# Kernel tuning notes

Measured on AMD Instinct MI355X. Metric: run time of the kernel, lower is better.

## Reference

```python
import jax, jax.numpy as jnp
import numpy as np

N_HEADS = 8
TOPK = 64
LN_EPS = 1e-5


def layernorm(x, g, b):
    mu = jnp.mean(x, axis=-1, keepdims=True)
    var = jnp.mean((x - mu) ** 2, axis=-1, keepdims=True)
    return (x - mu) * jax.lax.rsqrt(var + LN_EPS) * g + b


def mha(x, wq, wk, wv, wo, causal):
    # x: [B, S, H]; weights are torch nn.Linear style [out, in]
    B, S, H = x.shape
    hd = H // N_HEADS
    scale = 1.0 / np.sqrt(hd)

    def proj(w):
        return (x @ w.T).reshape(B, S, N_HEADS, hd).transpose(0, 2, 1, 3)  # [B, n, S, hd]

    q, k, v = proj(wq), proj(wk), proj(wv)
    s = jnp.einsum('bnqd,bnkd->bnqk', q, k) * scale
    if causal:
        m = jnp.tril(jnp.ones((S, S), bool))
        s = jnp.where(m, s, jnp.finfo(s.dtype).min)
    a = jax.nn.softmax(s, axis=-1)
    o = jnp.einsum('bnqk,bnkd->bnqd', a, v).transpose(0, 2, 1, 3).reshape(B, S, H)
    return o @ wo.T


def topk_activation(x, k):
    # x: [N, F]; keep top-k per row, zero elsewhere (matches topk + scatter_)
    vals, idx = jax.lax.top_k(x, k)
    rows = jnp.arange(x.shape[0])[:, None]
    return jnp.zeros_like(x).at[rows, idx].set(vals)


def setup_inputs() -> dict:
    key = jax.random.key(0)
    B, D, L, H, F = 8, 16, 128, 512, 4096
    ks = jax.random.split(key, 12)
    s = 1.0 / np.sqrt(H)
    w = lambda k, shp, sc: jax.random.normal(k, shp, jnp.float32) * sc
    return {
        'zL': w(ks[0], (B, D, L, H), 1.0),
        'wq_l': w(ks[1], (H, H), s), 'wk_l': w(ks[2], (H, H), s),
        'wv_l': w(ks[3], (H, H), s), 'wo_l': w(ks[4], (H, H), s),
        'gamma_l': jnp.ones(H, jnp.float32), 'beta_l': jnp.zeros(H, jnp.float32),
        'wq_d': w(ks[5], (H, H), s), 'wk_d': w(ks[6], (H, H), s),
        'wv_d': w(ks[7], (H, H), s), 'wo_d': w(ks[8], (H, H), s),
        'gamma_d': jnp.ones(H, jnp.float32), 'beta_d': jnp.zeros(H, jnp.float32),
        'dict_enc': w(ks[9], (F, H), np.sqrt(2.0 / (H + F))),
        'bias_pre': jnp.zeros(H, jnp.float32),
        'bias_enc': jnp.zeros(F, jnp.float32),
        'query_token': jnp.zeros(H, jnp.float32),
    }


def reference(zL, wq_l, wk_l, wv_l, wo_l, gamma_l, beta_l,
              wq_d, wk_d, wv_d, wo_d, gamma_d, beta_d,
              dict_enc, bias_pre, bias_enc, query_token):
    B, D, L, H = zL.shape
    F = dict_enc.shape[0]
    # prepend learned query token along depth, drop last layer
    qt = jnp.broadcast_to(query_token[None, None, None, :], (B, 1, L, H))
    x = jnp.concatenate([qt, zL[:, :-1, :, :]], axis=1)  # [B, D, L, H]
    # non-causal attention over L within each (b, d)
    x = x.reshape(B * D, L, H)
    x = x + mha(layernorm(x, gamma_l, beta_l), wq_l, wk_l, wv_l, wo_l, causal=False)
    # causal attention over D within each (b, l)
    x = x.reshape(B, D, L, H).transpose(0, 2, 1, 3).reshape(B * L, D, H)
    x = x + mha(layernorm(x, gamma_d, beta_d), wq_d, wk_d, wv_d, wo_d, causal=True)
    x_prior = x.reshape(B, L, D, H).transpose(0, 2, 1, 3)  # [B, D, L, H]
    # dictionary encode on residual (detached in original)
    N = B * D * L
    x_src = jax.lax.stop_gradient(zL - x_prior).reshape(N, H)
    logits = (x_src - bias_pre[None, :]) @ dict_enc.T + bias_enc
    z_dense = jax.nn.relu(logits)
    z_flat = topk_activation(z_dense, TOPK)
    z_n = z_flat.reshape(B, D, L, F)
    return z_n, x_prior
```

## Files before the change

### kernel.cpp

```cpp
#include <hip/hip_runtime.h>
#include <stdint.h>

#define NTOK 16384
#define HDIM 512
#define FDIM 4096
#define NHEAD 8
#define QKVD 1536
#define L2E 1.44269504f

typedef __attribute__((ext_vector_type(8))) _Float16 f16x8;
typedef __attribute__((ext_vector_type(16))) float f32x16;
#define LOSCALE 4096.0f
#define LOINV   (1.0f / 4096.0f)

static __device__ __forceinline__ void ld8f(const float* p, float* v) {
    *(float4*)&v[0] = *(const float4*)p;
    *(float4*)&v[4] = *(const float4*)(p + 4);
}
static __device__ __forceinline__ void st8f(float* p, const float* v) {
    *(float4*)p       = *(const float4*)&v[0];
    *(float4*)(p + 4) = *(const float4*)&v[4];
}

__global__ __launch_bounds__(256) void build_x_k(const float* __restrict__ zL,
                                                 const float* __restrict__ qt,
                                                 float* __restrict__ X) {
    int idx = blockIdx.x * 256 + threadIdx.x;
    int n = idx >> 6;
    int h = (idx & 63) << 3;
    int d = (n >> 7) & 15;
    const float* src = d ? (zL + (((size_t)(n - 128)) << 9) + h) : (qt + h);
    float v[8];
    ld8f(src, v);
    st8f(X + (((size_t)n) << 9) + h, v);
}

__global__ __launch_bounds__(256) void ln_split_k(const float* __restrict__ X,
                                                  const float* __restrict__ gamma,
                                                  const float* __restrict__ beta,
                                                  _Float16* __restrict__ ph,
                                                  _Float16* __restrict__ pl) {
    int row = blockIdx.x * 4 + (threadIdx.x >> 6);
    int lane = threadIdx.x & 63;
    int h = lane << 3;
    const float* xr = X + (((size_t)row) << 9) + h;
    float v[8];
    ld8f(xr, v);
    float s = 0.f;
#pragma unroll
    for (int i = 0; i < 8; ++i) s += v[i];
#pragma unroll
    for (int off = 32; off; off >>= 1) s += __shfl_xor(s, off);
    float m = s * (1.0f / 512.0f);
    float q = 0.f;
#pragma unroll
    for (int i = 0; i < 8; ++i) { float d = v[i] - m; q += d * d; }
#pragma unroll
    for (int off = 32; off; off >>= 1) q += __shfl_xor(q, off);
    float rs = 1.0f / sqrtf(q * (1.0f / 512.0f) + 1e-5f);
    float gv[8], be[8];
    ld8f(gamma + h, gv);
    ld8f(beta + h, be);
    _Float16 h8[8], l8[8];
#pragma unroll
    for (int i = 0; i < 8; ++i) {
        float y = (v[i] - m) * rs * gv[i] + be[i];
        _Float16 hh = (_Float16)y;
        h8[i] = hh;
        l8[i] = (_Float16)((y - (float)hh) * LOSCALE);
    }
    size_t off = (((size_t)row) << 9) + h;
    *(int4*)(ph + off) = *(int4*)h8;
    *(int4*)(pl + off) = *(int4*)l8;
}

__global__ __launch_bounds__(512) void attn_l_k(const float* __restrict__ QKV,
                                                _Float16* __restrict__ xh,
                                                _Float16* __restrict__ xl) {
    __shared__ float ks[64][64];
    __shared__ float vs[64][64];
    const int seq = blockIdx.x, head = blockIdx.y;
    const int t = threadIdx.x;
    const size_t tok0 = (size_t)seq << 7;
    const int ho = head << 6;
    const int r = t >> 2;
    const int q = t & 3;
    const float* qp = QKV + (tok0 + r) * QKVD + ho;
    float qr[16];
#pragma unroll
    for (int i = 0; i < 16; ++i) qr[i] = qp[(i << 2) + q];
    float o[16];
#pragma unroll
    for (int d = 0; d < 16; ++d) o[d] = 0.f;
    float m = -1e30f, l = 0.f;
    for (int half = 0; half < 2; ++half) {
        const int j0 = half << 6;
        __syncthreads();
#pragma unroll
        for (int i = 0; i < 2; ++i) {
            int slot = t + (i << 9);
            int row = slot >> 4;
            int c4 = (slot & 15) << 2;
            size_t g = (tok0 + j0 + row) * QKVD + ho + c4;
            *(float4*)&ks[row][c4] = *(const float4*)(QKV + g + 512);
            *(float4*)&vs[row][c4] = *(const float4*)(QKV + g + 1024);
        }
        __syncthreads();
        for (int j = 0; j < 64; ++j) {
            const float* kp = &ks[j][q];
            float s0 = 0.f, s1 = 0.f, s2 = 0.f, s3 = 0.f;
#pragma unroll
            for (int i = 0; i < 16; i += 4) {
                s0 = fmaf(qr[i + 0], kp[(i + 0) << 2], s0);
                s1 = fmaf(qr[i + 1], kp[(i + 1) << 2], s1);
                s2 = fmaf(qr[i + 2], kp[(i + 2) << 2], s2);
                s3 = fmaf(qr[i + 3], kp[(i + 3) << 2], s3);
            }
            float sp = (s0 + s1) + (s2 + s3);
            sp += __shfl_xor(sp, 1);
            sp += __shfl_xor(sp, 2);
            float s = sp * 0.125f;
            if (s > m) {
                float c = exp2f((m - s) * L2E);
#pragma unroll
                for (int d = 0; d < 16; ++d) o[d] *= c;
                l *= c;
                m = s;
            }
            float w = exp2f((s - m) * L2E);
            l += w;
            const float* vp = &vs[j][q];
#pragma unroll
            for (int i = 0; i < 16; ++i) o[i] = fmaf(w, vp[i << 2], o[i]);
        }
    }
    float inv = 1.0f / l;
    size_t eo = ((tok0 + r) << 9) + ho + q;
#pragma unroll
    for (int i = 0; i < 16; ++i) {
        float y = o[i] * inv;
        _Float16 hh = (_Float16)y;
        xh[eo + (i << 2)] = hh;
        xl[eo + (i << 2)] = (_Float16)((y - (float)hh) * LOSCALE);
    }
}

__global__ __launch_bounds__(128) void attn_d_k(const float* __restrict__ QKV,
                                                _Float16* __restrict__ xh,
                                                _Float16* __restrict__ xl) {
    __shared__ float ks[16][512];
    __shared__ float vs[16][512];
    const int bl = blockIdx.x;
    const int b = bl >> 7, l = bl & 127;
    const int t = threadIdx.x;
    const size_t tok0 = (size_t)b * 2048 + l;
#pragma unroll
    for (int i = 0; i < 16; ++i) {
        int c4 = t << 2;
        int hc = c4 >> 6;
        int p  = (c4 & ~63) | ((c4 + (hc << 2)) & 63);
        size_t g = (tok0 + (size_t)i * 128) * QKVD + c4;
        *(float4*)&ks[i][p] = *(const float4*)(QKV + g + 512);
        *(float4*)&vs[i][p] = *(const float4*)(QKV + g + 1024);
    }
    __syncthreads();
    const int head = t >> 4, dr = t & 15;
    const int ho = head << 6;
    const int rot = head << 2;
    float qr[64];
    const float* qp = QKV + (tok0 + (size_t)dr * 128) * QKVD + ho;
#pragma unroll
    for (int i = 0; i < 16; ++i) *(float4*)&qr[i << 2] = *(const float4*)(qp + (i << 2));
    float s[16];
    float m = -1e30f;
#pragma unroll
    for (int j = 0; j < 16; ++j) {
        float s0 = 0.f, s1 = 0.f, s2 = 0.f, s3 = 0.f;
#pragma unroll
        for (int d = 0; d < 64; d += 4) {
            s0 = fmaf(qr[d + 0], ks[j][ho + ((d + 0 + rot) & 63)], s0);
            s1 = fmaf(qr[d + 1], ks[j][ho + ((d + 1 + rot) & 63)], s1);
            s2 = fmaf(qr[d + 2], ks[j][ho + ((d + 2 + rot) & 63)], s2);
            s3 = fmaf(qr[d + 3], ks[j][ho + ((d + 3 + rot) & 63)], s3);
        }
        float sv = ((s0 + s1) + (s2 + s3)) * 0.125f;
        s[j] = (j <= dr) ? sv : -1e30f;
        m = fmaxf(m, s[j]);
    }
    float lsum = 0.f;
#pragma unroll
    for (int j = 0; j < 16; ++j) {
        float w = (j <= dr) ? exp2f((s[j] - m) * L2E) : 0.f;
        s[j] = w;
        lsum += w;
    }
    float inv = 1.0f / lsum;
    float o[64];
#pragma unroll
    for (int d = 0; d < 64; ++d) o[d] = 0.f;
#pragma unroll
    for (int j = 0; j < 16; ++j) {
        float w = s[j];
#pragma unroll
        for (int d = 0; d < 64; ++d) o[d] = fmaf(w, vs[j][ho + ((d + rot) & 63)], o[d]);
    }
    size_t eo = ((tok0 + (size_t)dr * 128) << 9) + ho;
#pragma unroll
    for (int i = 0; i < 8; ++i) {
        _Float16 h8[8], l8[8];
#pragma unroll
        for (int j = 0; j < 8; ++j) {
            float y = o[i * 8 + j] * inv;
            _Float16 hh = (_Float16)y;
            h8[j] = hh;
            l8[j] = (_Float16)((y - (float)hh) * LOSCALE);
        }
        *(int4*)(xh + eo + (i << 3)) = *(int4*)h8;
        *(int4*)(xl + eo + (i << 3)) = *(int4*)l8;
    }
}

__global__ __launch_bounds__(256) void xprior_xsrc_k(const float* __restrict__ zL,
                                                     const float* __restrict__ bias_pre,
                                                     const float* __restrict__ X,
                                                     float* __restrict__ out_xp,
                                                     _Float16* __restrict__ xh,
                                                     _Float16* __restrict__ xl) {
    int idx = blockIdx.x * 256 + threadIdx.x;
    int h = (idx & 63) << 3;
    size_t off = ((size_t)idx) << 3;
    float z[8], p[8], x[8];
    ld8f(zL + off, z);
    ld8f(bias_pre + h, p);
    ld8f(X + off, x);
    st8f(out_xp + off, x);
    _Float16 h8[8], l8[8];
#pragma unroll
    for (int i = 0; i < 8; ++i) {
        float y = z[i] - x[i] - p[i];
        _Float16 hh = (_Float16)y;
        h8[i] = hh;
        l8[i] = (_Float16)((y - (float)hh) * LOSCALE);
    }
    *(int4*)(xh + off) = *(int4*)h8;
    *(int4*)(xl + off) = *(int4*)l8;
}

__global__ __launch_bounds__(256) void split2_k(const float* __restrict__ in,
                                                _Float16* __restrict__ ph,
                                                _Float16* __restrict__ pl) {
    int idx = blockIdx.x * 256 + threadIdx.x;
    float v[8];
    ld8f(in + (((size_t)idx) << 3), v);
    _Float16 h8[8], l8[8];
#pragma unroll
    for (int i = 0; i < 8; ++i) {
        _Float16 h = (_Float16)v[i];
        float r = v[i] - (float)h;
        h8[i] = h;
        l8[i] = (_Float16)(r * LOSCALE);
    }
    *(int4*)(ph + (((size_t)idx) << 3)) = *(int4*)h8;
    *(int4*)(pl + (((size_t)idx) << 3)) = *(int4*)l8;
}

#define LDT 34
template<int SWZ, bool ADD_C, bool BIAS>
__global__ __launch_bounds__(256) void gemm_f16_k(
        const _Float16* __restrict__ Xh, const _Float16* __restrict__ Xl,
        const _Float16* __restrict__ Wh, const _Float16* __restrict__ Wl,
        const float* __restrict__ bias, float* __restrict__ Cout, int ldc) {
    __shared__ _Float16 Ah[2][128][LDT], Al[2][128][LDT];
    __shared__ _Float16 Bh[2][64][LDT],  Bl[2][64][LDT];
    const int tid = threadIdx.x;
    int bm, bn;
    if (SWZ) {
        int id = blockIdx.x;
        int xcd = id & 7, ww = id >> 3;
        bn = ((xcd << 3) | (ww & 7)) << 6;
        bm = (ww >> 3) << 7;
    } else {
        bm = blockIdx.y << 7;
        bn = blockIdx.x << 6;
    }
    const int w = tid >> 6, lane = tid & 63;
    const int wr = w >> 1, wc = w & 1;
    const int l31 = lane & 31, hh = lane >> 5;
    const int ar0 = tid >> 2, akg = (tid & 3) << 3;
    const int ar1 = ar0 + 64;
    const _Float16* pXh0 = Xh + (size_t)(bm + ar0) * HDIM + akg;
    const _Float16* pXl0 = Xl + (size_t)(bm + ar0) * HDIM + akg;
    const _Float16* pXh1 = Xh + (size_t)(bm + ar1) * HDIM + akg;
    const _Float16* pXl1 = Xl + (size_t)(bm + ar1) * HDIM + akg;
    const _Float16* pWh  = Wh + (size_t)(bn + ar0) * HDIM + akg;
    const _Float16* pWl  = Wl + (size_t)(bn + ar0) * HDIM + akg;

    f32x16 acc1[2], acc2[2];
#pragma unroll
    for (int i = 0; i < 2; ++i)
#pragma unroll
        for (int r = 0; r < 16; ++r) { acc1[i][r] = 0.f; acc2[i][r] = 0.f; }

    int4 ra0h, ra0l, ra1h, ra1l, rbh, rbl;
    auto LOADR = [&](int k0) {
        ra0h = *(const int4*)(pXh0 + k0);
        ra0l = *(const int4*)(pXl0 + k0);
        ra1h = *(const int4*)(pXh1 + k0);
        ra1l = *(const int4*)(pXl1 + k0);
        rbh  = *(const int4*)(pWh + k0);
        rbl  = *(const int4*)(pWl + k0);
    };
    auto STORE = [&](int buf) {
        *(int4*)&Ah[buf][ar0][akg] = ra0h;
        *(int4*)&Al[buf][ar0][akg] = ra0l;
        *(int4*)&Ah[buf][ar1][akg] = ra1h;
        *(int4*)&Al[buf][ar1][akg] = ra1l;
        *(int4*)&Bh[buf][ar0][akg] = rbh;
        *(int4*)&Bl[buf][ar0][akg] = rbl;
    };

    LOADR(0);
    STORE(0);
    int cur = 0;
    for (int it = 0; it < 16; ++it) {
        if (it < 15) LOADR((it + 1) << 5);
        __syncthreads();
#pragma unroll
        for (int kh = 0; kh < 2; ++kh) {
            const int ko = (kh << 4) + (hh << 3);
            f16x8 fah[2], fal[2];
#pragma unroll
            for (int mf = 0; mf < 2; ++mf) {
                int ar = (wr << 6) + (mf << 5) + l31;
                fah[mf] = *(const f16x8*)&Ah[cur][ar][ko];
                fal[mf] = *(const f16x8*)&Al[cur][ar][ko];
            }
            int bc_ = (wc << 5) + l31;
            f16x8 bh = *(const f16x8*)&Bh[cur][bc_][ko];
            f16x8 bl = *(const f16x8*)&Bl[cur][bc_][ko];
#pragma unroll
            for (int mf = 0; mf < 2; ++mf) {
                acc1[mf] = __builtin_amdgcn_mfma_f32_32x32x16_f16(fah[mf], bh, acc1[mf], 0, 0, 0);
                acc2[mf] = __builtin_amdgcn_mfma_f32_32x32x16_f16(fah[mf], bl, acc2[mf], 0, 0, 0);
                acc2[mf] = __builtin_amdgcn_mfma_f32_32x32x16_f16(fal[mf], bh, acc2[mf], 0, 0, 0);
            }
        }
        if (it < 15) { STORE(cur ^ 1); cur ^= 1; }
    }
    const int col = bn + (wc << 5) + l31;
    const float badd = BIAS ? bias[col] : 0.f;
#pragma unroll
    for (int mf = 0; mf < 2; ++mf) {
#pragma unroll
        for (int r = 0; r < 16; ++r) {
            int row = bm + (wr << 6) + (mf << 5) + (r & 3) + ((r >> 2) << 3) + (hh << 2);
            float* cp = Cout + (size_t)row * ldc + col;
            float val = acc1[mf][r] + acc2[mf][r] * LOINV + badd;
            if (ADD_C) val += *cp;
            *cp = val;
        }
    }
}

__global__ __launch_bounds__(256) void topk_k(const float* __restrict__ logits,
                                              float* __restrict__ out) {
    const int row = blockIdx.x;
    const float* lr = logits + (((size_t)row) << 12);
    const int t = threadIdx.x;
    float v[16]; uint32_t u[16];
#pragma unroll
    for (int i = 0; i < 16; ++i) {
        float x = fmaxf(lr[t + (i << 8)], 0.f);
        v[i] = x;
        u[i] = __float_as_uint(x);
    }
    __shared__ int red[4];
    __shared__ unsigned long long bits[64];
    __shared__ int s_cut;
    uint32_t prefix = 0;
    bool exact = false;
    for (int bit = 30; bit >= 0; --bit) {
        uint32_t c = prefix | (1u << bit);
        int cnt = 0;
#pragma unroll
        for (int i = 0; i < 16; ++i) cnt += (u[i] >= c) ? 1 : 0;
#pragma unroll
        for (int off = 32; off; off >>= 1) cnt += __shfl_xor(cnt, off);
        if ((t & 63) == 0) red[t >> 6] = cnt;
        __syncthreads();
        int total = red[0] + red[1] + red[2] + red[3];
        __syncthreads();
        if (total >= 64) prefix = c;
        if (total == 64) { exact = true; break; }
    }
    float* orow = out + (((size_t)row) << 12);
    if (exact) {
#pragma unroll
        for (int i = 0; i < 16; ++i) {
            int col = t + (i << 8);
            orow[col] = (u[i] >= prefix) ? v[i] : 0.f;
        }
        return;
    }
    const uint32_t T64 = prefix;
    int cg = 0;
#pragma unroll
    for (int i = 0; i < 16; ++i) cg += (u[i] > T64) ? 1 : 0;
#pragma unroll
    for (int off = 32; off; off >>= 1) cg += __shfl_xor(cg, off);
    if ((t & 63) == 0) red[t >> 6] = cg;
    __syncthreads();
    const int ngt = red[0] + red[1] + red[2] + red[3];
    int cut = -1;
    if (T64 != 0u) {
        const int r = 64 - ngt;
        if (t < 64) bits[t] = 0ull;
        __syncthreads();
#pragma unroll
        for (int i = 0; i < 16; ++i) {
            if (u[i] == T64) {
                int col = t + (i << 8);
                atomicOr(&bits[col >> 6], 1ull << (col & 63));
            }
        }
        __syncthreads();
        if (t == 0) {
            int need = r, cs = FDIM - 1;
            for (int wd = 0; wd < 64; ++wd) {
                int pc = __popcll(bits[wd]);
                if (need <= pc) {
                    unsigned long long bb = bits[wd];
                    for (int q = 1; q < need; ++q) bb &= bb - 1;
                    cs = (wd << 6) + (__ffsll(bb) - 1);
                    break;
                }
                need -= pc;
            }
            s_cut = cs;
        }
        __syncthreads();
        cut = s_cut;
    }
#pragma unroll
    for (int i = 0; i < 16; ++i) {
        int col = t + (i << 8);
        bool keep = (u[i] > T64) || (T64 != 0u && u[i] == T64 && col <= cut);
        orow[col] = keep ? v[i] : 0.f;
    }
}

extern "C" void kernel_launch(void* const* d_in, const int* in_sizes, int n_in,
                              void* d_out, int out_size, void* d_ws, size_t ws_size,
                              hipStream_t stream) {
    const float* zL      = (const float*)d_in[0];
    const float* gamma_l = (const float*)d_in[5];
    const float* beta_l  = (const float*)d_in[6];
    const float* gamma_d = (const float*)d_in[11];
    const float* beta_d  = (const float*)d_in[12];
    const float* dict_e  = (const float*)d_in[13];
    const float* bias_pre= (const float*)d_in[14];
    const float* bias_enc= (const float*)d_in[15];
    const float* qt      = (const float*)d_in[16];
    const float* wproj[8] = { (const float*)d_in[1], (const float*)d_in[2],
                              (const float*)d_in[3], (const float*)d_in[4],
                              (const float*)d_in[7], (const float*)d_in[8],
                              (const float*)d_in[9], (const float*)d_in[10] };

    float* out_z  = (float*)d_out;
    float* out_xp = out_z + (size_t)NTOK * FDIM;

    const size_t NHf = (size_t)NTOK * HDIM;
    float* B0 = (float*)d_out;
    float* B1 = B0 + NHf;

    float* wsf    = (float*)d_ws;
    float* logits = wsf + 64;

    const size_t dictE = (size_t)FDIM * HDIM;
    const size_t WE    = (size_t)HDIM * HDIM;

    int crows = 2048;
    const size_t fixedB = 64 * sizeof(float)
                        + (2 * dictE + 16 * WE + 2 * NHf) * sizeof(_Float16);
    while (crows > 128 && fixedB + (size_t)crows * FDIM * sizeof(float) > ws_size)
        crows >>= 1;

    _Float16* dh  = (_Float16*)(logits + (size_t)crows * FDIM);
    _Float16* dl  = dh + dictE;
    _Float16* wsp = dh + 2 * dictE;
    _Float16* xh  = wsp + 16 * WE;
    _Float16* xl  = xh + NHf;
    _Float16* qkvh_l = wsp;
    _Float16* qkvl_l = wsp + 3 * WE;
    _Float16* woh_l  = wsp + 6 * WE;
    _Float16* wol_l  = wsp + 7 * WE;
    _Float16* qkvh_d = wsp + 8 * WE;
    _Float16* qkvl_d = wsp + 11 * WE;
    _Float16* woh_d  = wsp + 14 * WE;
    _Float16* wol_d  = wsp + 15 * WE;

    const dim3 blk256(256), blk128(128), blk512(512);
    const dim3 gElem(4096);
    const dim3 gW(WE / 8 / 256);
    const dim3 gQKV(QKVD / 64, NTOK / 128);
    const dim3 gWo(HDIM / 64, NTOK / 128);

    split2_k<<<gW, blk256, 0, stream>>>(wproj[0], qkvh_l,          qkvl_l);
    split2_k<<<gW, blk256, 0, stream>>>(wproj[1], qkvh_l + WE,     qkvl_l + WE);
    split2_k<<<gW, blk256, 0, stream>>>(wproj[2], qkvh_l + 2 * WE, qkvl_l + 2 * WE);
    split2_k<<<gW, blk256, 0, stream>>>(wproj[3], woh_l,           wol_l);
    split2_k<<<gW, blk256, 0, stream>>>(wproj[4], qkvh_d,          qkvl_d);
    split2_k<<<gW, blk256, 0, stream>>>(wproj[5], qkvh_d + WE,     qkvl_d + WE);
    split2_k<<<gW, blk256, 0, stream>>>(wproj[6], qkvh_d + 2 * WE, qkvl_d + 2 * WE);
    split2_k<<<gW, blk256, 0, stream>>>(wproj[7], woh_d,           wol_d);
    split2_k<<<dim3(dictE / 8 / 256), blk256, 0, stream>>>(dict_e, dh, dl);

    build_x_k<<<gElem, blk256, 0, stream>>>(zL, qt, B0);

    ln_split_k<<<dim3(NTOK / 4), blk256, 0, stream>>>(B0, gamma_l, beta_l, xh, xl);
    gemm_f16_k<0, false, false><<<gQKV, blk256, 0, stream>>>(xh, xl, qkvh_l, qkvl_l, nullptr, B1, QKVD);
    attn_l_k<<<dim3(128, NHEAD), blk512, 0, stream>>>(B1, xh, xl);
    gemm_f16_k<0, true, false><<<gWo, blk256, 0, stream>>>(xh, xl, woh_l, wol_l, nullptr, B0, HDIM);

    ln_split_k<<<dim3(NTOK / 4), blk256, 0, stream>>>(B0, gamma_d, beta_d, xh, xl);
    gemm_f16_k<0, false, false><<<gQKV, blk256, 0, stream>>>(xh, xl, qkvh_d, qkvl_d, nullptr, B1, QKVD);
    attn_d_k<<<dim3(1024), blk128, 0, stream>>>(B1, xh, xl);
    gemm_f16_k<0, true, false><<<gWo, blk256, 0, stream>>>(xh, xl, woh_d, wol_d, nullptr, B0, HDIM);

    xprior_xsrc_k<<<gElem, blk256, 0, stream>>>(zL, bias_pre, B0, out_xp, xh, xl);

    for (int c0 = 0; c0 < NTOK; c0 += crows) {
        if ((crows & 127) == 0 && (crows / 128) * 64 % 8 == 0) {
            gemm_f16_k<1, false, true><<<dim3(64 * (crows / 128)), blk256, 0, stream>>>(
                xh + (size_t)c0 * HDIM, xl + (size_t)c0 * HDIM,
                dh, dl, bias_enc, logits, FDIM);
        } else {
            gemm_f16_k<0, false, true><<<dim3(FDIM / 64, crows / 128), blk256, 0, stream>>>(
                xh + (size_t)c0 * HDIM, xl + (size_t)c0 * HDIM,
                dh, dl, bias_enc, logits, FDIM);
        }
        topk_k<<<dim3(crows), blk256, 0, stream>>>(logits, out_z + (size_t)c0 * FDIM);
    }
}
```

Before: 1.166 ms.

## Rewrite L-axis attention with split-fp16 MFMA for QK^T and PV

Replaces the scalar FMA online-softmax attention over L with a block-wide MFMA version. Q, K and V are split into packed hi/lo fp16 pairs in LDS, scores are computed with 32x32x16 MFMAs using three products for near-fp32 accuracy, and a full-row softmax runs in LDS before a second MFMA pass for P·V. It removes the scalar dot-product and shuffle cost, in exchange for about 100KB of LDS per block, which limits occupancy, plus packing overhead and some loss of accuracy from the split.

```diff
diff --git a/kernel.cpp b/kernel.cpp
--- a/kernel.cpp
+++ b/kernel.cpp
@@ -20,6 +20,23 @@
 static __device__ __forceinline__ void st8f(float* p, const float* v) {
     *(float4*)p       = *(const float4*)&v[0];
     *(float4*)(p + 4) = *(const float4*)&v[4];
+}
+static __device__ __forceinline__ uint32_t packsplit(float v) {
+    _Float16 h = (_Float16)v;
+    _Float16 l = (_Float16)((v - (float)h) * LOSCALE);
+    union { _Float16 f; uint16_t u; } ch{h}, cl{l};
+    return (uint32_t)ch.u | ((uint32_t)cl.u << 16);
+}
+static __device__ __forceinline__ void unpack8(const uint32_t* p, f16x8* h, f16x8* l) {
+    union { uint16_t s[8]; f16x8 v; } uh, ul;
+#pragma unroll
+    for (int i = 0; i < 8; ++i) {
+        uint32_t x = p[i];
+        uh.s[i] = (uint16_t)(x & 0xffffu);
+        ul.s[i] = (uint16_t)(x >> 16);
+    }
+    *h = uh.v;
+    *l = ul.v;
 }
 
 __global__ __launch_bounds__(256) void build_x_k(const float* __restrict__ zL,
@@ -74,75 +91,137 @@
     *(int4*)(pl + off) = *(int4*)l8;
 }
 
-__global__ __launch_bounds__(512) void attn_l_k(const float* __restrict__ QKV,
+__global__ __launch_bounds__(256) void attn_l_k(const float* __restrict__ QKV,
                                                 _Float16* __restrict__ xh,
                                                 _Float16* __restrict__ xl) {
-    __shared__ float ks[64][64];
-    __shared__ float vs[64][64];
+    __shared__ uint32_t pool[25024];
+    uint32_t* Qp = pool;
+    uint32_t* Kp = pool + 8320;
+    uint32_t* Vt = pool + 16640;
+    float*    rl = (float*)(pool + 24896);
+    uint32_t* S  = pool;
+
     const int seq = blockIdx.x, head = blockIdx.y;
     const int t = threadIdx.x;
     const size_t tok0 = (size_t)seq << 7;
     const int ho = head << 6;
-    const int r = t >> 2;
-    const int q = t & 3;
-    const float* qp = QKV + (tok0 + r) * QKVD + ho;
-    float qr[16];
-#pragma unroll
-    for (int i = 0; i < 16; ++i) qr[i] = qp[(i << 2) + q];
-    float o[16];
-#pragma unroll
-    for (int d = 0; d < 16; ++d) o[d] = 0.f;
-    float m = -1e30f, l = 0.f;
-    for (int half = 0; half < 2; ++half) {
-        const int j0 = half << 6;
-        __syncthreads();
-#pragma unroll
-        for (int i = 0; i < 2; ++i) {
-            int slot = t + (i << 9);
-            int row = slot >> 4;
-            int c4 = (slot & 15) << 2;
-            size_t g = (tok0 + j0 + row) * QKVD + ho + c4;
-            *(float4*)&ks[row][c4] = *(const float4*)(QKV + g + 512);
-            *(float4*)&vs[row][c4] = *(const float4*)(QKV + g + 1024);
-        }
-        __syncthreads();
+    const int w = t >> 6, lane = t & 63;
+    const int wr = w >> 1, wc = w & 1;
+    const int l31 = lane & 31, hh = lane >> 5;
+
+#pragma unroll
+    for (int i = 0; i < 8; ++i) {
+        int idx = t + (i << 8);
+        int row = idx >> 4, c4 = (idx & 15) << 2;
+        size_t g = (tok0 + row) * QKVD + ho + c4;
+        float4 qv = *(const float4*)(QKV + g);
+        float4 kv = *(const float4*)(QKV + g + 512);
+        float4 vv = *(const float4*)(QKV + g + 1024);
+        uint32_t* qd = Qp + row * 65 + c4;
+        qd[0] = packsplit(qv.x); qd[1] = packsplit(qv.y);
+        qd[2] = packsplit(qv.z); qd[3] = packsplit(qv.w);
+        uint32_t* kd = Kp + row * 65 + c4;
+        kd[0] = packsplit(kv.x); kd[1] = packsplit(kv.y);
+        kd[2] = packsplit(kv.z); kd[3] = packsplit(kv.w);
+        Vt[(c4 + 0) * 129 + row] = packsplit(vv.x);
+        Vt[(c4 + 1) * 129 + row] = packsplit(vv.y);
+        Vt[(c4 + 2) * 129 + row] = packsplit(vv.z);
+        Vt[(c4 + 3) * 129 + row] = packsplit(vv.w);
+    }
+    __syncthreads();
+
+    f32x16 a1[2][2], a2[2][2];
+#pragma unroll
+    for (int i = 0; i < 2; ++i)
+#pragma unroll
+        for (int j = 0; j < 2; ++j)
+#pragma unroll
+            for (int r = 0; r < 16; ++r) { a1[i][j][r] = 0.f; a2[i][j][r] = 0.f; }
+#pragma unroll
+    for (int ks = 0; ks < 4; ++ks) {
+        const int ko = (ks << 4) + (hh << 3);
+        f16x8 qh[2], ql[2], kh[2], kl[2];
+#pragma unroll
+        for (int mf = 0; mf < 2; ++mf)
+            unpack8(Qp + ((wr << 6) + (mf << 5) + l31) * 65 + ko, &qh[mf], &ql[mf]);
+#pragma unroll
+        for (int nf = 0; nf < 2; ++nf)
+            unpack8(Kp + ((wc << 6) + (nf << 5) + l31) * 65 + ko, &kh[nf], &kl[nf]);
+#pragma unroll
+        for (int nf = 0; nf < 2; ++nf)
+#pragma unroll
+            for (int mf = 0; mf < 2; ++mf) {
+                a1[mf][nf] = __builtin_amdgcn_mfma_f32_32x32x16_f16(qh[mf], kh[nf], a1[mf][nf], 0, 0, 0);
+                a2[mf][nf] = __builtin_amdgcn_mfma_f32_32x32x16_f16(qh[mf], kl[nf], a2[mf][nf], 0, 0, 0);
+                a2[mf][nf] = __builtin_amdgcn_mfma_f32_32x32x16_f16(ql[mf], kh[nf], a2[mf][nf], 0, 0, 0);
+            }
+    }
+    __syncthreads();
+#pragma unroll
+    for (int mf = 0; mf < 2; ++mf)
+#pragma unroll
+        for (int nf = 0; nf < 2; ++nf) {
+            int col = (wc << 6) + (nf << 5) + l31;
+#pragma unroll
+            for (int r = 0; r < 16; ++r) {
+                int row = (wr << 6) + (mf << 5) + (r & 3) + ((r >> 2) << 3) + (hh << 2);
+                float sv = (a1[mf][nf][r] + a2[mf][nf][r] * LOINV) * 0.125f;
+                S[row * 129 + col] = __float_as_uint(sv);
+            }
+        }
+    __syncthreads();
+
+    {
+        int row = t >> 1, half = t & 1;
+        uint32_t* sr = S + row * 129 + (half << 6);
+        float mx = -1e30f;
+#pragma unroll
+        for (int j = 0; j < 64; ++j) mx = fmaxf(mx, __uint_as_float(sr[j]));
+        mx = fmaxf(mx, __shfl_xor(mx, 1));
+        float sum = 0.f;
+#pragma unroll
         for (int j = 0; j < 64; ++j) {
-            const float* kp = &ks[j][q];
-            float s0 = 0.f, s1 = 0.f, s2 = 0.f, s3 = 0.f;
-#pragma unroll
-            for (int i = 0; i < 16; i += 4) {
-                s0 = fmaf(qr[i + 0], kp[(i + 0) << 2], s0);
-                s1 = fmaf(qr[i + 1], kp[(i + 1) << 2], s1);
-                s2 = fmaf(qr[i + 2], kp[(i + 2) << 2], s2);
-                s3 = fmaf(qr[i + 3], kp[(i + 3) << 2], s3);
-            }
-            float sp = (s0 + s1) + (s2 + s3);
-            sp += __shfl_xor(sp, 1);
-            sp += __shfl_xor(sp, 2);
-            float s = sp * 0.125f;
-            if (s > m) {
-                float c = exp2f((m - s) * L2E);
-#pragma unroll
-                for (int d = 0; d < 16; ++d) o[d] *= c;
-                l *= c;
-                m = s;
-            }
-            float w = exp2f((s - m) * L2E);
-            l += w;
-            const float* vp = &vs[j][q];
-#pragma unroll
-            for (int i = 0; i < 16; ++i) o[i] = fmaf(w, vp[i << 2], o[i]);
-        }
-    }
-    float inv = 1.0f / l;
-    size_t eo = ((tok0 + r) << 9) + ho + q;
-#pragma unroll
-    for (int i = 0; i < 16; ++i) {
-        float y = o[i] * inv;
-        _Float16 hh = (_Float16)y;
-        xh[eo + (i << 2)] = hh;
-        xl[eo + (i << 2)] = (_Float16)((y - (float)hh) * LOSCALE);
-    }
+            float wg = exp2f((__uint_as_float(sr[j]) - mx) * L2E);
+            sum += wg;
+            sr[j] = packsplit(wg);
+        }
+        sum += __shfl_xor(sum, 1);
+        if (!half) rl[row] = 1.0f / sum;
+    }
+    __syncthreads();
+
+    f32x16 o1[2], o2[2];
+#pragma unroll
+    for (int i = 0; i < 2; ++i)
+#pragma unroll
+        for (int r = 0; r < 16; ++r) { o1[i][r] = 0.f; o2[i][r] = 0.f; }
+    const int dcol = (wc << 5) + l31;
+#pragma unroll
+    for (int ks = 0; ks < 8; ++ks) {
+        const int jo = (ks << 4) + (hh << 3);
+        f16x8 ph[2], pl2[2], vh, vl;
+#pragma unroll
+        for (int mf = 0; mf < 2; ++mf)
+            unpack8(S + ((wr << 6) + (mf << 5) + l31) * 129 + jo, &ph[mf], &pl2[mf]);
+        unpack8(Vt + dcol * 129 + jo, &vh, &vl);
+#pragma unroll
+        for (int mf = 0; mf < 2; ++mf) {
+            o1[mf] = __builtin_amdgcn_mfma_f32_32x32x16_f16(ph[mf], vh, o1[mf], 0, 0, 0);
+            o2[mf] = __builtin_amdgcn_mfma_f32_32x32x16_f16(ph[mf], vl, o2[mf], 0, 0, 0);
+            o2[mf] = __builtin_amdgcn_mfma_f32_32x32x16_f16(pl2[mf], vh, o2[mf], 0, 0, 0);
+        }
+    }
+#pragma unroll
+    for (int mf = 0; mf < 2; ++mf)
+#pragma unroll
+        for (int r = 0; r < 16; ++r) {
+            int row = (wr << 6) + (mf << 5) + (r & 3) + ((r >> 2) << 3) + (hh << 2);
+            float y = (o1[mf][r] + o2[mf][r] * LOINV) * rl[row];
+            size_t eo = ((tok0 + row) << 9) + ho + dcol;
+            _Float16 hv = (_Float16)y;
+            xh[eo] = hv;
+            xl[eo] = (_Float16)((y - (float)hv) * LOSCALE);
+        }
 }
 
 __global__ __launch_bounds__(128) void attn_d_k(const float* __restrict__ QKV,
@@ -499,7 +578,7 @@
     _Float16* woh_d  = wsp + 14 * WE;
     _Float16* wol_d  = wsp + 15 * WE;
 
-    const dim3 blk256(256), blk128(128), blk512(512);
+    const dim3 blk256(256), blk128(128);
     const dim3 gElem(4096);
     const dim3 gW(WE / 8 / 256);
     const dim3 gQKV(QKVD / 64, NTOK / 128);
@@ -519,7 +598,7 @@
 
     ln_split_k<<<dim3(NTOK / 4), blk256, 0, stream>>>(B0, gamma_l, beta_l, xh, xl);
     gemm_f16_k<0, false, false><<<gQKV, blk256, 0, stream>>>(xh, xl, qkvh_l, qkvl_l, nullptr, B1, QKVD);
-    attn_l_k<<<dim3(128, NHEAD), blk512, 0, stream>>>(B1, xh, xl);
+    attn_l_k<<<dim3(128, NHEAD), blk256, 0, stream>>>(B1, xh, xl);
     gemm_f16_k<0, true, false><<<gWo, blk256, 0, stream>>>(xh, xl, woh_l, wol_l, nullptr, B0, HDIM);
 
     ln_split_k<<<dim3(NTOK / 4), blk256, 0, stream>>>(B0, gamma_d, beta_d, xh, xl);
```

Measured after the change: 1.067 ms. 8.5% less time.
